# Performance work log

Hardware: AMD Instinct MI355X
Metric: run time of the kernel (lower is better)

Reference implementation:

```python
import jax, jax.numpy as jnp
import numpy as np

B, Q, N0, N1, N2 = 2, 16, 4096, 1024, 256
DIM, CTX, HEADS = 296, 288, 8
I1, I2, I3 = 144, 72, 36
EPS = 1e-5  # BatchNorm eps (eval mode)


def setup_inputs():
    key = jax.random.key(0)
    ks = iter(jax.random.split(key, 64))
    def rn(shape, scale=1.0):
        return scale * jax.random.normal(next(ks), shape, dtype=jnp.float32)
    def ru(shape, lo, hi):
        return jax.random.uniform(next(ks), shape, dtype=jnp.float32, minval=lo, maxval=hi)
    def bn(c):  # rows: gamma, beta, running_mean, running_var
        return jnp.stack([1.0 + 0.1 * rn((c,)), 0.1 * rn((c,)), 0.1 * rn((c,)), 1.0 + 0.1 * jnp.abs(rn((c,)))])
    def lin(o, i):
        s = 1.0 / np.sqrt(i)
        return rn((o, i), s), rn((o,), s)
    w1, b1 = lin(DIM, DIM); w2, b2 = lin(I1, DIM)
    a1_w, a1_b = lin(I2, 3); a2_w, a2_b = lin(I1, 128)
    fp1_w1, fp1_b1 = lin(I1, 2 * I1); fp1_w2, fp1_b2 = lin(I2, I1)
    fp2_w1, fp2_b1 = lin(I2, 2 * I2); fp2_w2, fp2_b2 = lin(I3, I2)
    out_w, out_b = lin(1, I3)
    return {
        "x": rn((B, CTX, N2)),
        "bbox_mask": ru((B, Q, HEADS, N2), 0.0, 1.0),
        "sa0_features": rn((B, 3, N0)),
        "sa1_features": rn((B, 128, N1)),
        "sa0_xyz": ru((B, N0, 3), -1.0, 1.0),
        "sa1_xyz": ru((B, N1, 3), -1.0, 1.0),
        "sa2_xyz": ru((B, N2, 3), -1.0, 1.0),
        "w1": w1, "b1": b1, "bn1": bn(DIM),
        "w2": w2, "b2": b2, "bn2": bn(I1),
        "a1_w": a1_w, "a1_b": a1_b,
        "a2_w": a2_w, "a2_b": a2_b,
        "fp1_w1": fp1_w1, "fp1_b1": fp1_b1, "fp1_bn1": bn(I1),
        "fp1_w2": fp1_w2, "fp1_b2": fp1_b2, "fp1_bn2": bn(I2),
        "fp2_w1": fp2_w1, "fp2_b1": fp2_b1, "fp2_bn1": bn(I2),
        "fp2_w2": fp2_w2, "fp2_b2": fp2_b2, "fp2_bn2": bn(I3),
        "out_w": out_w, "out_b": out_b,
    }


def _expand(t, q):
    # tensor.unsqueeze(1).repeat(1, q, 1, 1).flatten(0, 1)
    b = t.shape[0]
    return jnp.broadcast_to(t[:, None], (b, q) + t.shape[1:]).reshape((b * q,) + t.shape[1:])


def _bn(x, p):
    g, b, m, v = p  # (C,) each; x: (BQ, C, N)
    return (x - m[:, None]) * (g * jax.lax.rsqrt(v + EPS))[:, None] + b[:, None]


def _layer(x, W, b, p):
    # SharedMLP layer: 1x1 Conv2d + BN(eval) + ReLU on (BQ, C, N[, 1])
    return jax.nn.relu(_bn(jnp.einsum('oc,bcn->bon', W, x) + b[None, :, None], p))


def _three_interpolate(unknown_xyz, known_xyz, known_feats):
    # three_nn: squared dists (BQ, Nu, Nk) -> 3 smallest; inverse-distance weights
    d2 = jnp.sum((unknown_xyz[:, :, None, :] - known_xyz[:, None, :, :]) ** 2, axis=-1)
    neg_d, idx = jax.lax.top_k(-d2, 3)
    w = 1.0 / (-neg_d + 1e-8)
    w = w / jnp.sum(w, axis=-1, keepdims=True)  # (BQ, Nu, 3)
    g = jax.vmap(lambda f, i: f[:, i])(known_feats, idx)  # (BQ, C, Nu, 3)
    return jnp.sum(g * w[:, None], axis=-1)  # (BQ, C, Nu)


def reference(x, bbox_mask, sa0_features, sa1_features, sa0_xyz, sa1_xyz, sa2_xyz, w1, b1, bn1, w2, b2, bn2, a1_w, a1_b, a2_w, a2_b, fp1_w1, fp1_b1, fp1_bn1, fp1_w2, fp1_b2, fp1_bn2, fp2_w1, fp2_b1, fp2_bn1, fp2_w2, fp2_b2, fp2_bn2, out_w, out_b):
    q = bbox_mask.shape[1]
    h = jnp.concatenate([_expand(x, q), bbox_mask.reshape((-1,) + bbox_mask.shape[2:])], axis=1)  # (BQ, DIM, N2)
    h = _layer(h, w1, b1, bn1)
    h = _layer(h, w2, b2, bn2)  # (BQ, I1, N2)
    f0 = jnp.einsum('oc,bcn->bon', a1_w, sa0_features) + a1_b[None, :, None]  # adapter1
    f1 = jnp.einsum('oc,bcn->bon', a2_w, sa1_features) + a2_b[None, :, None]  # adapter2
    f0, f1 = _expand(f0, q), _expand(f1, q)
    xyz0, xyz1, xyz2 = _expand(sa0_xyz, q), _expand(sa1_xyz, q), _expand(sa2_xyz, q)
    # FP1: propagate sa2 -> sa1, concat [interpolated, skip] as in PointnetFPModule
    h = jnp.concatenate([_three_interpolate(xyz1, xyz2, h), f1], axis=1)
    h = _layer(h, fp1_w1, fp1_b1, fp1_bn1)
    h = _layer(h, fp1_w2, fp1_b2, fp1_bn2)
    # FP2: propagate sa1 -> sa0
    h = jnp.concatenate([_three_interpolate(xyz0, xyz1, h), f0], axis=1)
    h = _layer(h, fp2_w1, fp2_b1, fp2_bn1)
    h = _layer(h, fp2_w2, fp2_b2, fp2_bn2)  # (BQ, I3, N0)
    out = jnp.einsum('oc,bcn->bon', out_w, h) + out_b[None, :, None]  # (BQ, 1, N0)
    return out
```

## Files before the change

kernel.cpp:

```cpp
#include <hip/hip_runtime.h>

#define EPS_BN 1e-5f
typedef float v2f __attribute__((ext_vector_type(2)));

struct LayerDesc {
    const float* W; const float* b; const float* bn;
    float* wt; float* shb; int O; int C;
};
struct HeadArgs {
    LayerDesc l[6];
    const float* a2w; const float* a2b; const float* w3; const float* b3; const float* bn3;
    float* w3c; float* sh3;
    const float* a1w; const float* a1b; const float* w5; const float* b5; const float* bn5;
    float* w5c; float* sh5;
    const float* xyz0; const float* xyz1; const float* xyz2;
    int* idx1; float* wgt1; int* idx2; float* wgt2;
};

__global__ __launch_bounds__(256) void head_kernel(HeadArgs a) {
    const int bx = blockIdx.x, tid = threadIdx.x;
    if (bx < 96) {
        LayerDesc d = a.l[bx / 16];
        int sub = bx % 16;
        int total = d.O * d.C;
        for (int i = sub * 256 + tid; i < total; i += 16 * 256) {
            int c = i / d.O, o = i - (i / d.O) * d.O;
            float sc = 1.f;
            if (d.bn) { float g = d.bn[o], v = d.bn[3 * d.O + o]; sc = g * rsqrtf(v + EPS_BN); }
            d.wt[i] = d.W[(size_t)o * d.C + c] * sc;
        }
        for (int o = sub * 256 + tid; o < d.O; o += 16 * 256) {
            float sc = 1.f, sh = 0.f;
            if (d.bn) {
                float g = d.bn[o], be = d.bn[d.O + o], m = d.bn[2 * d.O + o], v = d.bn[3 * d.O + o];
                sc = g * rsqrtf(v + EPS_BN); sh = be - m * sc;
            }
            d.shb[o] = d.b[o] * sc + sh;
        }
        return;
    } else if (bx < 169) {
        int e = (bx - 96) * 256 + tid;
        if (e < 128 * 144) {
            int k = e / 144, o = e - (e / 144) * 144;
            float sc = a.bn3[o] * rsqrtf(a.bn3[3 * 144 + o] + EPS_BN);
            float s = 0.f;
            for (int c = 0; c < 144; ++c)
                s += a.a2w[c * 128 + k] * a.w3[(size_t)o * 288 + 144 + c];
            a.w3c[k * 144 + o] = s * sc;
        } else if (e < 128 * 144 + 144) {
            int o = e - 128 * 144;
            float g = a.bn3[o], be = a.bn3[144 + o], m = a.bn3[2 * 144 + o], v = a.bn3[3 * 144 + o];
            float sc = g * rsqrtf(v + EPS_BN);
            float s = 0.f;
            for (int c = 0; c < 144; ++c) s += a.w3[(size_t)o * 288 + 144 + c] * a.a2b[c];
            a.sh3[o] = (s + a.b3[o] - m) * sc + be;
        }
        return;
    } else if (bx < 171) {
        int e = (bx - 169) * 256 + tid;
        if (e < 3 * 72) {
            int k = e / 72, o = e - (e / 72) * 72;
            float sc = a.bn5[o] * rsqrtf(a.bn5[3 * 72 + o] + EPS_BN);
            float s = 0.f;
            for (int c = 0; c < 72; ++c)
                s += a.a1w[c * 3 + k] * a.w5[(size_t)o * 144 + 72 + c];
            a.w5c[k * 72 + o] = s * sc;
        } else if (e < 3 * 72 + 72) {
            int o = e - 3 * 72;
            float g = a.bn5[o], be = a.bn5[72 + o], m = a.bn5[2 * 72 + o], v = a.bn5[3 * 72 + o];
            float sc = g * rsqrtf(v + EPS_BN);
            float s = 0.f;
            for (int c = 0; c < 72; ++c) s += a.w5[(size_t)o * 144 + 72 + c] * a.a1b[c];
            a.sh5[o] = (s + a.b5[o] - m) * sc + be;
        }
        return;
    }
    const int NSEG = 8;
    __shared__ float kl[3 * 1024];
    __shared__ float sd[NSEG][32][3];
    __shared__ int   si[NSEG][32][3];
    const float* unknown; const float* known;
    int Nu, Nk, blk, b; int* idx; float* wgt;
    int t = bx - 171;
    if (t < 64) {
        unknown = a.xyz1; known = a.xyz2; Nu = 1024; Nk = 256;
        b = t >> 5; blk = t & 31; idx = a.idx1; wgt = a.wgt1;
    } else {
        t -= 64;
        unknown = a.xyz0; known = a.xyz1; Nu = 4096; Nk = 1024;
        b = t >> 7; blk = t & 127; idx = a.idx2; wgt = a.wgt2;
    }
    for (int i = tid; i < Nk * 3; i += 256) kl[i] = known[(size_t)b * Nk * 3 + i];
    __syncthreads();
    const int u   = tid & 31;
    const int seg = tid >> 5;
    const int n   = blk * 32 + u;
    const float* up = unknown + ((size_t)b * Nu + n) * 3;
    const float ux = up[0], uy = up[1], uz = up[2];
    float d0 = 1e30f, d1 = 1e30f, d2 = 1e30f;
    int i0 = 0, i1 = 0, i2 = 0;
    const int klo = seg * (Nk / NSEG), khi = klo + Nk / NSEG;
    for (int k = klo; k < khi; ++k) {
        float dx = __fsub_rn(ux, kl[3 * k + 0]);
        float dy = __fsub_rn(uy, kl[3 * k + 1]);
        float dz = __fsub_rn(uz, kl[3 * k + 2]);
        float d = __fadd_rn(__fadd_rn(__fmul_rn(dx, dx), __fmul_rn(dy, dy)), __fmul_rn(dz, dz));
        if (d < d0)      { d2 = d1; i2 = i1; d1 = d0; i1 = i0; d0 = d; i0 = k; }
        else if (d < d1) { d2 = d1; i2 = i1; d1 = d;  i1 = k; }
        else if (d < d2) { d2 = d;  i2 = k; }
    }
    sd[seg][u][0] = d0; sd[seg][u][1] = d1; sd[seg][u][2] = d2;
    si[seg][u][0] = i0; si[seg][u][1] = i1; si[seg][u][2] = i2;
    __syncthreads();
    if (tid < 32) {
        float m0 = 1e30f, m1 = 1e30f, m2 = 1e30f;
        int j0 = 0, j1 = 0, j2 = 0;
        for (int s = 0; s < NSEG; ++s)
            for (int c = 0; c < 3; ++c) {
                float d = sd[s][u][c];
                int ii = si[s][u][c];
                if (d < m0)      { m2 = m1; j2 = j1; m1 = m0; j1 = j0; m0 = d; j0 = ii; }
                else if (d < m1) { m2 = m1; j2 = j1; m1 = d;  j1 = ii; }
                else if (d < m2) { m2 = d;  j2 = ii; }
            }
        float w0 = 1.f / (m0 + 1e-8f), w1 = 1.f / (m1 + 1e-8f), w2 = 1.f / (m2 + 1e-8f);
        float s = w0 + w1 + w2;
        size_t base = ((size_t)b * Nu + n) * 3;
        idx[base + 0] = j0; idx[base + 1] = j1; idx[base + 2] = j2;
        wgt[base + 0] = w0 / s; wgt[base + 1] = w1 / s; wgt[base + 2] = w2 / s;
    }
}

template <int CTW>
__device__ __forceinline__ void conv_kloop(
    const float* __restrict__ s0, int N, const float* wldsw, v2f (&acc)[4][2])
{
    static_assert(CTW % 8 == 0 || CTW % 8 == 4, "CT tail");
    auto loadrow = [&](float (&x)[4], int c) {
        float4 t = *reinterpret_cast<const float4*>(s0 + (size_t)c * N);
        x[0] = t.x; x[1] = t.y; x[2] = t.z; x[3] = t.w;
    };
    auto comprow = [&](const float (&x)[4], int c) {
        v2f x01; x01[0] = x[0]; x01[1] = x[1];
        v2f x23; x23[0] = x[2]; x23[1] = x[3];
        float4 wv = *reinterpret_cast<const float4*>(wldsw + c * 4);
        float ww[4] = {wv.x, wv.y, wv.z, wv.w};
#pragma unroll
        for (int r = 0; r < 4; ++r) {
            v2f w2; w2[0] = ww[r]; w2[1] = ww[r];
            acc[r][0] = __builtin_elementwise_fma(w2, x01, acc[r][0]);
            acc[r][1] = __builtin_elementwise_fma(w2, x23, acc[r][1]);
        }
    };
    auto loadg = [&](float (&buf)[4][4], int c) {
#pragma unroll
        for (int q = 0; q < 4; ++q) loadrow(buf[q], c + q);
    };
    auto compg = [&](const float (&buf)[4][4], int c) {
#pragma unroll
        for (int q = 0; q < 4; ++q) comprow(buf[q], c + q);
    };
    float xa[4][4], xb[4][4];
    loadg(xa, 0); loadg(xb, 4);
    int c = 0;
#pragma unroll 1
    for (; c + 16 <= CTW; c += 8) {
        compg(xa, c);     loadg(xa, c + 8);
        compg(xb, c + 4); loadg(xb, c + 12);
    }
    compg(xa, c);
    if constexpr (CTW % 8 == 4) {
        loadg(xa, c + 8);
        compg(xb, c + 4);
        compg(xa, c + 8);
    } else {
        compg(xb, c + 4);
    }
}

template <int CT0, int CT1, int O, bool RELU, int ADD, bool TOUT>
__device__ __forceinline__ void conv2w(
    int nt, int ot, int nb, int tid,
    const float* __restrict__ src0, int qdiv0,
    const float* __restrict__ Wt, const float* __restrict__ shb,
    const float* __restrict__ basep, int qdivb,
    float* __restrict__ outp, int N, float* wlds, float* sred)
{
    constexpr int CTALL = CT0 + CT1;
    const int wid = tid >> 6, lane = tid & 63;
    const int oBase = ot * 4;
    const int n0 = (nt * 64 + lane) * 4;

    for (int i = tid; i < CTALL * 4; i += 128)
        wlds[i] = Wt[(size_t)(i >> 2) * O + oBase + (i & 3)];
    __syncthreads();

    const int c0 = wid ? CT0 : 0;
    const float* s0 = src0 + (size_t)(nb / qdiv0) * CTALL * N + (size_t)c0 * N + n0;

    v2f acc[4][2];
#pragma unroll
    for (int r = 0; r < 4; ++r) { acc[r][0] = (v2f)0.f; acc[r][1] = (v2f)0.f; }

    if (wid == 0) conv_kloop<CT0>(s0, N, wlds, acc);
    else          conv_kloop<CT1>(s0, N, wlds + CT0 * 4, acc);

    if (wid == 1) {
#pragma unroll
        for (int i = 0; i < 16; ++i)
            sred[i * 64 + lane] = acc[i >> 2][(i >> 1) & 1][i & 1];
    }
    __syncthreads();
    if (wid != 0) return;
#pragma unroll
    for (int i = 0; i < 16; ++i)
        acc[i >> 2][(i >> 1) & 1][i & 1] += sred[i * 64 + lane];

    if constexpr (TOUT) {
#pragma unroll
        for (int j = 0; j < 4; ++j) {
            float4 t;
            t.x = acc[0][j >> 1][j & 1];
            t.y = acc[1][j >> 1][j & 1];
            t.z = acc[2][j >> 1][j & 1];
            t.w = acc[3][j >> 1][j & 1];
            *reinterpret_cast<float4*>(outp + ((size_t)nb * N + n0 + j) * O + oBase) = t;
        }
        return;
    }
    const float* bp = (ADD == 2) ? (basep + ((size_t)(nb / qdivb) * O + oBase) * N + n0) : nullptr;
#pragma unroll
    for (int ol = 0; ol < 4; ++ol) {
        int o = oBase + ol;
        float addv[4];
        if constexpr (ADD == 2) {
            float4 t = *reinterpret_cast<const float4*>(bp + (size_t)ol * N);
            addv[0] = t.x; addv[1] = t.y; addv[2] = t.z; addv[3] = t.w;
        } else if constexpr (ADD == 1) {
            float sb = shb[o];
#pragma unroll
            for (int j = 0; j < 4; ++j) addv[j] = sb;
        } else {
#pragma unroll
            for (int j = 0; j < 4; ++j) addv[j] = 0.f;
        }
        float res[4];
#pragma unroll
        for (int j = 0; j < 4; ++j) {
            float y = acc[ol][j >> 1][j & 1] + addv[j];
            if constexpr (RELU) y = fmaxf(y, 0.f);
            res[j] = y;
        }
        float4 t; t.x = res[0]; t.y = res[1]; t.z = res[2]; t.w = res[3];
        *reinterpret_cast<float4*>(outp + ((size_t)nb * O + o) * N + n0) = t;
    }
}

template <int CT0, int CT1, int O, bool RELU, int ADD, bool TOUT>
__global__ __launch_bounds__(128) void conv_ks2(
    const float* __restrict__ src0, int qdiv0,
    const float* __restrict__ Wt, const float* __restrict__ shb,
    const float* __restrict__ basep, int qdivb,
    float* __restrict__ outp, int N, int GX, int GY)
{
    __shared__ __align__(16) float wlds[(CT0 + CT1) * 4];
    __shared__ float sred[16 * 64];
    int f = blockIdx.x;
    int J = gridDim.x >> 3;
    int j = (f & 7) * J + (f >> 3);
    int ot = j % GY; int r = j / GY;
    int nt = r % GX; int nb = r / GX;
    conv2w<CT0, CT1, O, RELU, ADD, TOUT>(
        nt, ot, nb, threadIdx.x, src0, qdiv0, Wt, shb, basep, qdivb, outp, N, wlds, sred);
}

template <int CT, int O, int OT, bool RELU, int ADD>
__global__ __launch_bounds__(64) void conv_swz(
    const float* __restrict__ src0, int qdiv0,
    const float* __restrict__ Wt, const float* __restrict__ shb,
    const float* __restrict__ basep, int qdivb,
    float* __restrict__ outp, int N, int GX, int GY)
{
    __shared__ __align__(16) float wlds[CT * OT];
    int f = blockIdx.x;
    int J = gridDim.x >> 3;
    int j = (f & 7) * J + (f >> 3);
    int ot = j % GY; int r = j / GY;
    int nt = r % GX; int nb = r / GX;
    const int lane = threadIdx.x;
    const int oBase = ot * OT;
    const int n0 = (nt * 64 + lane) * 4;
    for (int i = lane; i < CT * OT; i += 64)
        wlds[i] = Wt[(size_t)(i / OT) * O + oBase + (i % OT)];
    __builtin_amdgcn_wave_barrier();
    const float* s0 = src0 + (size_t)(nb / qdiv0) * CT * N + n0;
    v2f acc[OT][2];
#pragma unroll
    for (int ol = 0; ol < OT; ++ol) { acc[ol][0] = (v2f)0.f; acc[ol][1] = (v2f)0.f; }
#pragma unroll
    for (int c = 0; c < CT; ++c) {
        float4 t = *reinterpret_cast<const float4*>(s0 + (size_t)c * N);
        v2f x01; x01[0] = t.x; x01[1] = t.y;
        v2f x23; x23[0] = t.z; x23[1] = t.w;
#pragma unroll
        for (int g = 0; g < OT / 4; ++g) {
            float4 wv = *reinterpret_cast<const float4*>(&wlds[c * OT + g * 4]);
            float ww[4] = {wv.x, wv.y, wv.z, wv.w};
#pragma unroll
            for (int r = 0; r < 4; ++r) {
                v2f w2; w2[0] = ww[r]; w2[1] = ww[r];
                acc[g * 4 + r][0] = __builtin_elementwise_fma(w2, x01, acc[g * 4 + r][0]);
                acc[g * 4 + r][1] = __builtin_elementwise_fma(w2, x23, acc[g * 4 + r][1]);
            }
        }
    }
    const float* bp = (ADD == 2) ? (basep + ((size_t)(nb / qdivb) * O + oBase) * N + n0) : nullptr;
#pragma unroll
    for (int ol = 0; ol < OT; ++ol) {
        int o = oBase + ol;
        float addv[4];
        if constexpr (ADD == 2) {
            float4 t = *reinterpret_cast<const float4*>(bp + (size_t)ol * N);
            addv[0] = t.x; addv[1] = t.y; addv[2] = t.z; addv[3] = t.w;
        } else if constexpr (ADD == 1) {
            float sb = shb[o];
#pragma unroll
            for (int j = 0; j < 4; ++j) addv[j] = sb;
        } else {
#pragma unroll
            for (int j = 0; j < 4; ++j) addv[j] = 0.f;
        }
        float res[4];
#pragma unroll
        for (int j = 0; j < 4; ++j) {
            float y = acc[ol][j >> 1][j & 1] + addv[j];
            if constexpr (RELU) y = fmaxf(y, 0.f);
            res[j] = y;
        }
        float4 t; t.x = res[0]; t.y = res[1]; t.z = res[2]; t.w = res[3];
        *reinterpret_cast<float4*>(outp + ((size_t)nb * O + o) * N + n0) = t;
    }
}

__global__ __launch_bounds__(128) void bases_kernel(
    const float* __restrict__ x, const float* __restrict__ sa1f,
    const float* __restrict__ wt1, const float* __restrict__ sb1,
    const float* __restrict__ w3c, const float* __restrict__ sh3,
    float* __restrict__ base1, float* __restrict__ base3)
{
    __shared__ __align__(16) float wlds[288 * 4];
    __shared__ float sred[16 * 64];
    const int bx = blockIdx.x, tid = threadIdx.x;
    if (bx < 148) {
        int ot = bx % 74, nb = bx / 74;
        conv2w<144, 144, 296, false, 1, false>(0, ot, nb, tid, x, 1, wt1, sb1, nullptr, 1, base1, 256, wlds, sred);
    } else {
        int lb = bx - 148;
        int nt = lb % 4, ot = (lb / 4) % 36, nb = lb / 144;
        conv2w<64, 64, 144, false, 1, false>(nt, ot, nb, tid, sa1f, 1, w3c, sh3, nullptr, 1, base3, 1024, wlds, sred);
    }
}

__global__ __launch_bounds__(64) void gather_t1_kernel(
    const float* __restrict__ g3t,
    const int* __restrict__ idx, const float* __restrict__ wgt,
    const float* __restrict__ base3,
    float* __restrict__ h3)
{
    int f = blockIdx.x;
    int j = (f & 7) * 128 + (f >> 3);
    int cseg = j & 1; int rest = j >> 1;
    int nb = rest >> 4, nt = rest & 15;
    int lane = threadIdx.x;
    int n = nt * 64 + lane;
    int b = nb >> 4;
    size_t nn = ((size_t)b * 1024 + n) * 3;
    int j0 = idx[nn], j1 = idx[nn + 1], j2 = idx[nn + 2];
    float w0 = wgt[nn], w1 = wgt[nn + 1], w2 = wgt[nn + 2];
    const float* gbase = g3t + (size_t)nb * 256 * 144;
    const float* p0 = gbase + (size_t)j0 * 144;
    const float* p1 = gbase + (size_t)j1 * 144;
    const float* p2 = gbase + (size_t)j2 * 144;
    const float* bb = base3 + (size_t)b * 144 * 1024 + n;
    float* ob = h3 + (size_t)nb * 144 * 1024 + n;
    const int cs = cseg * 72;
#pragma unroll 1
    for (int cc = cs; cc < cs + 72; cc += 8) {
        float4 a0 = *reinterpret_cast<const float4*>(p0 + cc);
        float4 a0b = *reinterpret_cast<const float4*>(p0 + cc + 4);
        float4 a1 = *reinterpret_cast<const float4*>(p1 + cc);
        float4 a1b = *reinterpret_cast<const float4*>(p1 + cc + 4);
        float4 a2 = *reinterpret_cast<const float4*>(p2 + cc);
        float4 a2b = *reinterpret_cast<const float4*>(p2 + cc + 4);
        float r0[8] = {a0.x, a0.y, a0.z, a0.w, a0b.x, a0b.y, a0b.z, a0b.w};
        float r1[8] = {a1.x, a1.y, a1.z, a1.w, a1b.x, a1b.y, a1b.z, a1b.w};
        float r2[8] = {a2.x, a2.y, a2.z, a2.w, a2b.x, a2b.y, a2b.z, a2b.w};
#pragma unroll
        for (int r = 0; r < 8; ++r) {
            float v = w0 * r0[r] + w1 * r1[r] + w2 * r2[r] + bb[(size_t)(cc + r) * 1024];
            ob[(size_t)(cc + r) * 1024] = fmaxf(v, 0.f);
        }
    }
}

__global__ __launch_bounds__(64) void h6out_kernel(
    const float* __restrict__ g5t,
    const int* __restrict__ idx, const float* __restrict__ wgt,
    const float* __restrict__ sa0,
    const float* __restrict__ w5c, const float* __restrict__ sh5,
    const float* __restrict__ Wt6, const float* __restrict__ shb6,
    const float* __restrict__ wout, const float* __restrict__ bout,
    float* __restrict__ outp)
{
    __shared__ __align__(16) float wlds[72 * 36];
    __shared__ float w5l[3 * 72];
    __shared__ float sh5l[72], ow[36], sh6l[36];
    const int tid = threadIdx.x;
    for (int i = tid; i < 72 * 36; i += 64) wlds[i] = Wt6[i];
    for (int i = tid; i < 216; i += 64) w5l[i] = w5c[i];
    for (int i = tid; i < 72; i += 64) sh5l[i] = sh5[i];
    if (tid < 36) { ow[tid] = wout[tid]; sh6l[tid] = shb6[tid]; }
    __syncthreads();
    int f = blockIdx.x;
    int j = (f & 7) * ((int)gridDim.x >> 3) + (f >> 3);
    const int nb = j >> 6;
    const int nt = j & 63;
    const int n = nt * 64 + tid;
    const int b = nb >> 4;
    size_t nn = ((size_t)b * 4096 + n) * 3;
    const int j0 = idx[nn], j1 = idx[nn + 1], j2 = idx[nn + 2];
    const float w0 = wgt[nn], w1 = wgt[nn + 1], w2 = wgt[nn + 2];
    const float* gbase = g5t + (size_t)nb * 1024 * 72;
    const float* p0 = gbase + (size_t)j0 * 72;
    const float* p1 = gbase + (size_t)j1 * 72;
    const float* p2 = gbase + (size_t)j2 * 72;
    const float* s0 = sa0 + (size_t)b * 3 * 4096 + n;
    const float sx = s0[0], sy = s0[4096], sz = s0[8192];

    v2f acc[18];
#pragma unroll
    for (int o = 0; o < 18; ++o) acc[o] = (v2f)0.f;

    float ra[8][3], rb[8][3];
    auto ld = [&](float (&r)[8][3], int c) {
        float4 a0 = *reinterpret_cast<const float4*>(p0 + c);
        float4 a0b = *reinterpret_cast<const float4*>(p0 + c + 4);
        float4 a1 = *reinterpret_cast<const float4*>(p1 + c);
        float4 a1b = *reinterpret_cast<const float4*>(p1 + c + 4);
        float4 a2 = *reinterpret_cast<const float4*>(p2 + c);
        float4 a2b = *reinterpret_cast<const float4*>(p2 + c + 4);
        r[0][0] = a0.x; r[1][0] = a0.y; r[2][0] = a0.z; r[3][0] = a0.w;
        r[4][0] = a0b.x; r[5][0] = a0b.y; r[6][0] = a0b.z; r[7][0] = a0b.w;
        r[0][1] = a1.x; r[1][1] = a1.y; r[2][1] = a1.z; r[3][1] = a1.w;
        r[4][1] = a1b.x; r[5][1] = a1b.y; r[6][1] = a1b.z; r[7][1] = a1b.w;
        r[0][2] = a2.x; r[1][2] = a2.y; r[2][2] = a2.z; r[3][2] = a2.w;
        r[4][2] = a2b.x; r[5][2] = a2b.y; r[6][2] = a2b.z; r[7][2] = a2b.w;
    };
    auto cp = [&](const float (&r)[8][3], int c) {
#pragma unroll
        for (int q = 0; q < 8; ++q) {
            int cc = c + q;
            float base = w5l[cc] * sx + w5l[72 + cc] * sy + w5l[144 + cc] * sz + sh5l[cc];
            float xv = fmaxf(w0 * r[q][0] + w1 * r[q][1] + w2 * r[q][2] + base, 0.f);
            v2f xv2; xv2[0] = xv; xv2[1] = xv;
#pragma unroll
            for (int g = 0; g < 9; ++g) {
                float4 wv = *reinterpret_cast<const float4*>(&wlds[cc * 36 + g * 4]);
                v2f wa; wa[0] = wv.x; wa[1] = wv.y;
                v2f wb; wb[0] = wv.z; wb[1] = wv.w;
                acc[g * 2 + 0] = __builtin_elementwise_fma(wa, xv2, acc[g * 2 + 0]);
                acc[g * 2 + 1] = __builtin_elementwise_fma(wb, xv2, acc[g * 2 + 1]);
            }
        }
    };
    ld(ra, 0); ld(rb, 8);
    int c = 0;
#pragma unroll 1
    for (; c + 32 <= 72; c += 16) {
        cp(ra, c);     ld(ra, c + 16);
        cp(rb, c + 8); ld(rb, c + 24);
    }
    cp(ra, 48); ld(ra, 64);
    cp(rb, 56);
    cp(ra, 64);

    float r = bout[0];
#pragma unroll
    for (int o = 0; o < 36; ++o) r += ow[o] * fmaxf(acc[o >> 1][o & 1] + sh6l[o], 0.f);
    outp[(size_t)nb * 4096 + n] = r;
}

extern "C" void kernel_launch(void* const* d_in, const int* in_sizes, int n_in,
                              void* d_out, int out_size, void* d_ws, size_t ws_size,
                              hipStream_t stream) {
    const int B = 2, Q = 16, N0 = 4096, N1 = 1024, N2 = 256;
    const int I1 = 144;
    const int NB = B * Q;

    const float* x     = (const float*)d_in[0];
    const float* mask  = (const float*)d_in[1];
    const float* sa0f  = (const float*)d_in[2];
    const float* sa1f  = (const float*)d_in[3];
    const float* xyz0  = (const float*)d_in[4];
    const float* xyz1  = (const float*)d_in[5];
    const float* xyz2  = (const float*)d_in[6];

    float* ws = (float*)d_ws;
    size_t off = 0;
    auto alloc = [&](size_t n) { size_t p = off; off += (n + 15) & ~(size_t)15; return p; };

    size_t wgt1  = alloc((size_t)B * N1 * 3);
    size_t wgt2  = alloc((size_t)B * N0 * 3);
    size_t idx1  = alloc((size_t)B * N1 * 3);
    size_t idx2  = alloc((size_t)B * N0 * 3);
    size_t slotA = alloc((size_t)NB * 296 * N2);
    size_t slotB = alloc((size_t)NB * I1 * N1);
    size_t base1 = alloc((size_t)B * 296 * N2);
    size_t base3 = alloc((size_t)B * I1 * N1);
    size_t wt1 = alloc(296 * 296), sb1 = alloc(296);
    size_t wt2 = alloc(296 * 144), sb2 = alloc(144);
    size_t wt3 = alloc(288 * 144), sb3 = alloc(144);
    size_t wt4 = alloc(144 * 72),  sb4 = alloc(72);
    size_t wt5 = alloc(144 * 72),  sb5 = alloc(72);
    size_t wt6 = alloc(72 * 36),   sb6 = alloc(36);
    size_t w3c = alloc(128 * 144), sh3 = alloc(144);
    size_t w5c = alloc(3 * 72),    sh5 = alloc(72);
    (void)ws_size; (void)in_sizes; (void)n_in;

    auto din = [&](int i) { return (const float*)d_in[i]; };

    HeadArgs ha;
    ha.l[0] = { din(7),  din(8),  din(9),  ws + wt1, ws + sb1, 296, 296 };
    ha.l[1] = { din(10), din(11), din(12), ws + wt2, ws + sb2, 144, 296 };
    ha.l[2] = { din(17), din(18), din(19), ws + wt3, ws + sb3, 144, 288 };
    ha.l[3] = { din(20), din(21), din(22), ws + wt4, ws + sb4, 72, 144 };
    ha.l[4] = { din(23), din(24), din(25), ws + wt5, ws + sb5, 72, 144 };
    ha.l[5] = { din(26), din(27), din(28), ws + wt6, ws + sb6, 36, 72 };
    ha.a2w = din(15); ha.a2b = din(16); ha.w3 = din(17); ha.b3 = din(18); ha.bn3 = din(19);
    ha.w3c = ws + w3c; ha.sh3 = ws + sh3;
    ha.a1w = din(13); ha.a1b = din(14); ha.w5 = din(23); ha.b5 = din(24); ha.bn5 = din(25);
    ha.w5c = ws + w5c; ha.sh5 = ws + sh5;
    ha.xyz0 = xyz0; ha.xyz1 = xyz1; ha.xyz2 = xyz2;
    ha.idx1 = (int*)(ws + idx1); ha.wgt1 = ws + wgt1;
    ha.idx2 = (int*)(ws + idx2); ha.wgt2 = ws + wgt2;
    head_kernel<<<dim3(171 + 64 + 256), 256, 0, stream>>>(ha);

    bases_kernel<<<dim3(436), 128, 0, stream>>>(
        x, sa1f, ws + wt1, ws + sb1, ws + w3c, ws + sh3, ws + base1, ws + base3);

    conv_swz<8, 296, 4, true, 2><<<dim3(2368), 64, 0, stream>>>(
        mask, 1, ws + wt1 + 288 * 296, ws + sb1, ws + base1, Q, ws + slotA, N2, 1, 74);

    conv_ks2<152, 144, 144, true, 1, false><<<dim3(1152), 128, 0, stream>>>(
        ws + slotA, 1, ws + wt2, ws + sb2, nullptr, 1, ws + slotB, N2, 1, 36);

    conv_ks2<72, 72, 144, false, 0, true><<<dim3(1152), 128, 0, stream>>>(
        ws + slotB, 1, ws + wt3, ws + sb3, nullptr, 1, ws + slotA, N2, 1, 36);

    gather_t1_kernel<<<dim3(1024), 64, 0, stream>>>(
        ws + slotA, (const int*)(ws + idx1), ws + wgt1, ws + base3, ws + slotB);

    conv_ks2<72, 72, 72, true, 1, false><<<dim3(2304), 128, 0, stream>>>(
        ws + slotB, 1, ws + wt4, ws + sb4, nullptr, 1, ws + slotA, N1, 4, 18);

    conv_ks2<36, 36, 72, false, 0, true><<<dim3(2304), 128, 0, stream>>>(
        ws + slotA, 1, ws + wt5, ws + sb5, nullptr, 1, ws + slotB, N1, 4, 18);

    h6out_kernel<<<dim3(2048), 64, 0, stream>>>(
        ws + slotB, (const int*)(ws + idx2), ws + wgt2, sa0f,
        ws + w5c, ws + sh5, ws + wt6, ws + sb6, din(29), din(30), (float*)d_out);
}
```

Measured before the change: 162.5 us.

## Split conv K-loops across four waves and h6out across two waves

The conv kernels move from a 2-wave to a 4-wave split-K, with the partial sums reduced through shared memory. h6out also splits its channel loop across two waves with an LDS reduction. This is meant to raise the number of waves in flight and shorten each wave's serial dependency chain on these small, latency-bound convolutions. In exchange it adds more LDS traffic and barriers for the reduction and uses larger shared-memory buffers, which may lower occupancy.

```diff
diff --git a/kernel.cpp b/kernel.cpp
--- a/kernel.cpp
+++ b/kernel.cpp
@@ -178,43 +178,46 @@
     }
 }
 
-template <int CT0, int CT1, int O, bool RELU, int ADD, bool TOUT>
-__device__ __forceinline__ void conv2w(
+template <int CA, int CB, int CC, int CD, int O, bool RELU, int ADD, bool TOUT>
+__device__ __forceinline__ void conv4w(
     int nt, int ot, int nb, int tid,
     const float* __restrict__ src0, int qdiv0,
     const float* __restrict__ Wt, const float* __restrict__ shb,
     const float* __restrict__ basep, int qdivb,
     float* __restrict__ outp, int N, float* wlds, float* sred)
 {
-    constexpr int CTALL = CT0 + CT1;
+    constexpr int CT = CA + CB + CC + CD;
     const int wid = tid >> 6, lane = tid & 63;
     const int oBase = ot * 4;
     const int n0 = (nt * 64 + lane) * 4;
 
-    for (int i = tid; i < CTALL * 4; i += 128)
+    for (int i = tid; i < CT * 4; i += 256)
         wlds[i] = Wt[(size_t)(i >> 2) * O + oBase + (i & 3)];
     __syncthreads();
 
-    const int c0 = wid ? CT0 : 0;
-    const float* s0 = src0 + (size_t)(nb / qdiv0) * CTALL * N + (size_t)c0 * N + n0;
+    const float* sbase = src0 + (size_t)(nb / qdiv0) * CT * N + n0;
 
     v2f acc[4][2];
 #pragma unroll
     for (int r = 0; r < 4; ++r) { acc[r][0] = (v2f)0.f; acc[r][1] = (v2f)0.f; }
 
-    if (wid == 0) conv_kloop<CT0>(s0, N, wlds, acc);
-    else          conv_kloop<CT1>(s0, N, wlds + CT0 * 4, acc);
-
-    if (wid == 1) {
+    if (wid == 0)      conv_kloop<CA>(sbase, N, wlds, acc);
+    else if (wid == 1) conv_kloop<CB>(sbase + (size_t)CA * N, N, wlds + CA * 4, acc);
+    else if (wid == 2) conv_kloop<CC>(sbase + (size_t)(CA + CB) * N, N, wlds + (CA + CB) * 4, acc);
+    else               conv_kloop<CD>(sbase + (size_t)(CA + CB + CC) * N, N, wlds + (CA + CB + CC) * 4, acc);
+
+    if (wid) {
 #pragma unroll
         for (int i = 0; i < 16; ++i)
-            sred[i * 64 + lane] = acc[i >> 2][(i >> 1) & 1][i & 1];
+            sred[(wid - 1) * 1024 + i * 64 + lane] = acc[i >> 2][(i >> 1) & 1][i & 1];
     }
     __syncthreads();
     if (wid != 0) return;
 #pragma unroll
-    for (int i = 0; i < 16; ++i)
-        acc[i >> 2][(i >> 1) & 1][i & 1] += sred[i * 64 + lane];
+    for (int w = 0; w < 3; ++w)
+#pragma unroll
+        for (int i = 0; i < 16; ++i)
+            acc[i >> 2][(i >> 1) & 1][i & 1] += sred[w * 1024 + i * 64 + lane];
 
     if constexpr (TOUT) {
 #pragma unroll
@@ -256,21 +259,21 @@
     }
 }
 
-template <int CT0, int CT1, int O, bool RELU, int ADD, bool TOUT>
-__global__ __launch_bounds__(128) void conv_ks2(
+template <int CA, int CB, int CC, int CD, int O, bool RELU, int ADD, bool TOUT>
+__global__ __launch_bounds__(256) void conv_ks4(
     const float* __restrict__ src0, int qdiv0,
     const float* __restrict__ Wt, const float* __restrict__ shb,
     const float* __restrict__ basep, int qdivb,
     float* __restrict__ outp, int N, int GX, int GY)
 {
-    __shared__ __align__(16) float wlds[(CT0 + CT1) * 4];
-    __shared__ float sred[16 * 64];
+    __shared__ __align__(16) float wlds[(CA + CB + CC + CD) * 4];
+    __shared__ float sred[3 * 16 * 64];
     int f = blockIdx.x;
     int J = gridDim.x >> 3;
     int j = (f & 7) * J + (f >> 3);
     int ot = j % GY; int r = j / GY;
     int nt = r % GX; int nb = r / GX;
-    conv2w<CT0, CT1, O, RELU, ADD, TOUT>(
+    conv4w<CA, CB, CC, CD, O, RELU, ADD, TOUT>(
         nt, ot, nb, threadIdx.x, src0, qdiv0, Wt, shb, basep, qdivb, outp, N, wlds, sred);
 }
 
@@ -342,22 +345,22 @@
     }
 }
 
-__global__ __launch_bounds__(128) void bases_kernel(
+__global__ __launch_bounds__(256) void bases_kernel(
     const float* __restrict__ x, const float* __restrict__ sa1f,
     const float* __restrict__ wt1, const float* __restrict__ sb1,
     const float* __restrict__ w3c, const float* __restrict__ sh3,
     float* __restrict__ base1, float* __restrict__ base3)
 {
     __shared__ __align__(16) float wlds[288 * 4];
-    __shared__ float sred[16 * 64];
+    __shared__ float sred[3 * 16 * 64];
     const int bx = blockIdx.x, tid = threadIdx.x;
     if (bx < 148) {
         int ot = bx % 74, nb = bx / 74;
-        conv2w<144, 144, 296, false, 1, false>(0, ot, nb, tid, x, 1, wt1, sb1, nullptr, 1, base1, 256, wlds, sred);
+        conv4w<72, 72, 72, 72, 296, false, 1, false>(0, ot, nb, tid, x, 1, wt1, sb1, nullptr, 1, base1, 256, wlds, sred);
     } else {
         int lb = bx - 148;
         int nt = lb % 4, ot = (lb / 4) % 36, nb = lb / 144;
-        conv2w<64, 64, 144, false, 1, false>(nt, ot, nb, tid, sa1f, 1, w3c, sh3, nullptr, 1, base3, 1024, wlds, sred);
+        conv4w<32, 32, 32, 32, 144, false, 1, false>(nt, ot, nb, tid, sa1f, 1, w3c, sh3, nullptr, 1, base3, 1024, wlds, sred);
     }
 }
 
@@ -403,7 +406,7 @@
     }
 }
 
-__global__ __launch_bounds__(64) void h6out_kernel(
+__global__ __launch_bounds__(128) void h6out_kernel(
     const float* __restrict__ g5t,
     const int* __restrict__ idx, const float* __restrict__ wgt,
     const float* __restrict__ sa0,
@@ -415,17 +418,19 @@
     __shared__ __align__(16) float wlds[72 * 36];
     __shared__ float w5l[3 * 72];
     __shared__ float sh5l[72], ow[36], sh6l[36];
+    __shared__ float sred[36 * 64];
     const int tid = threadIdx.x;
-    for (int i = tid; i < 72 * 36; i += 64) wlds[i] = Wt6[i];
-    for (int i = tid; i < 216; i += 64) w5l[i] = w5c[i];
-    for (int i = tid; i < 72; i += 64) sh5l[i] = sh5[i];
+    for (int i = tid; i < 72 * 36; i += 128) wlds[i] = Wt6[i];
+    for (int i = tid; i < 216; i += 128) w5l[i] = w5c[i];
+    if (tid < 72) sh5l[tid] = sh5[tid];
     if (tid < 36) { ow[tid] = wout[tid]; sh6l[tid] = shb6[tid]; }
     __syncthreads();
     int f = blockIdx.x;
     int j = (f & 7) * ((int)gridDim.x >> 3) + (f >> 3);
     const int nb = j >> 6;
     const int nt = j & 63;
-    const int n = nt * 64 + tid;
+    const int wid = tid >> 6, lane = tid & 63;
+    const int n = nt * 64 + lane;
     const int b = nb >> 4;
     size_t nn = ((size_t)b * 4096 + n) * 3;
     const int j0 = idx[nn], j1 = idx[nn + 1], j2 = idx[nn + 2];
@@ -473,16 +478,25 @@
             }
         }
     };
-    ld(ra, 0); ld(rb, 8);
-    int c = 0;
+    const int cs = wid ? 40 : 0;
+    const int ce = wid ? 72 : 40;
+    ld(ra, cs);
 #pragma unroll 1
-    for (; c + 32 <= 72; c += 16) {
-        cp(ra, c);     ld(ra, c + 16);
-        cp(rb, c + 8); ld(rb, c + 24);
-    }
-    cp(ra, 48); ld(ra, 64);
-    cp(rb, 56);
-    cp(ra, 64);
+    for (int cc = cs; cc < ce; cc += 16) {
+        if (cc + 8 < ce) ld(rb, cc + 8);
+        cp(ra, cc);
+        if (cc + 16 < ce) ld(ra, cc + 16);
+        if (cc + 8 < ce) cp(rb, cc + 8);
+    }
+
+    if (wid == 1) {
+#pragma unroll
+        for (int i = 0; i < 36; ++i) sred[i * 64 + lane] = acc[i >> 1][i & 1];
+    }
+    __syncthreads();
+    if (wid != 0) return;
+#pragma unroll
+    for (int i = 0; i < 36; ++i) acc[i >> 1][i & 1] += sred[i * 64 + lane];
 
     float r = bout[0];
 #pragma unroll
@@ -545,28 +559,28 @@
     ha.idx2 = (int*)(ws + idx2); ha.wgt2 = ws + wgt2;
     head_kernel<<<dim3(171 + 64 + 256), 256, 0, stream>>>(ha);
 
-    bases_kernel<<<dim3(436), 128, 0, stream>>>(
+    bases_kernel<<<dim3(436), 256, 0, stream>>>(
         x, sa1f, ws + wt1, ws + sb1, ws + w3c, ws + sh3, ws + base1, ws + base3);
 
     conv_swz<8, 296, 4, true, 2><<<dim3(2368), 64, 0, stream>>>(
         mask, 1, ws + wt1 + 288 * 296, ws + sb1, ws + base1, Q, ws + slotA, N2, 1, 74);
 
-    conv_ks2<152, 144, 144, true, 1, false><<<dim3(1152), 128, 0, stream>>>(
+    conv_ks4<80, 72, 72, 72, 144, true, 1, false><<<dim3(1152), 256, 0, stream>>>(
         ws + slotA, 1, ws + wt2, ws + sb2, nullptr, 1, ws + slotB, N2, 1, 36);
 
-    conv_ks2<72, 72, 144, false, 0, true><<<dim3(1152), 128, 0, stream>>>(
+    conv_ks4<36, 36, 36, 36, 144, false, 0, true><<<dim3(1152), 256, 0, stream>>>(
         ws + slotB, 1, ws + wt3, ws + sb3, nullptr, 1, ws + slotA, N2, 1, 36);
 
     gather_t1_kernel<<<dim3(1024), 64, 0, stream>>>(
         ws + slotA, (const int*)(ws + idx1), ws + wgt1, ws + base3, ws + slotB);
 
-    conv_ks2<72, 72, 72, true, 1, false><<<dim3(2304), 128, 0, stream>>>(
+    conv_ks4<36, 36, 36, 36, 72, true, 1, false><<<dim3(2304), 256, 0, stream>>>(
         ws + slotB, 1, ws + wt4, ws + sb4, nullptr, 1, ws + slotA, N1, 4, 18);
 
-    conv_ks2<36, 36, 72, false, 0, true><<<dim3(2304), 128, 0, stream>>>(
+    conv_ks4<20, 20, 16, 16, 72, false, 0, true><<<dim3(2304), 256, 0, stream>>>(
         ws + slotA, 1, ws + wt5, ws + sb5, nullptr, 1, ws + slotB, N1, 4, 18);
 
-    h6out_kernel<<<dim3(2048), 64, 0, stream>>>(
+    h6out_kernel<<<dim3(2048), 128, 0, stream>>>(
         ws + slotB, (const int*)(ws + idx2), ws + wgt2, sa0f,
         ws + w5c, ws + sh5, ws + wt6, ws + sb6, din(29), din(30), (float*)d_out);
 }
```

Result: slower. 178.3 us (+9.7%).
